# Kernel optimization log

Hardware: AMD Instinct MI355X
Metric: run time of the kernel (lower is better)

## Reference

```python
import jax, jax.numpy as jnp
import numpy as np

N_PROPOSALS = 100000
N_LABELS = 256
IOU_THRESHOLD = 0.5
FPS = 25.0


def setup_inputs() -> dict:
    key = jax.random.key(0)
    k1, k2, k3, k4, k5 = jax.random.split(key, 5)
    conf = jax.random.uniform(k1, (N_PROPOSALS,), dtype=jnp.float32)
    p_start = jax.random.uniform(k2, (N_PROPOSALS,), dtype=jnp.float32) * 2500.0  # frames
    p_len = jax.random.uniform(k3, (N_PROPOSALS,), dtype=jnp.float32) * 250.0 + 1.0
    proposals = jnp.stack([conf, p_start, p_start + p_len], axis=1)  # [N,3]
    l_start = jax.random.uniform(k4, (N_LABELS,), dtype=jnp.float32) * 100.0  # seconds
    l_len = jax.random.uniform(k5, (N_LABELS,), dtype=jnp.float32) * 10.0 + 0.5
    labels = jnp.stack([l_start, l_start + l_len], axis=1)  # [M,2]
    return {"proposals": proposals, "labels": labels}


def _iou_matrix(proposals, labels):
    # iou_with_anchors, vectorized over proposals (rows) x labels (cols)
    a_min = proposals[:, 1] / FPS  # [N] seconds
    a_max = proposals[:, 2] / FPS
    b_min = labels[:, 0]  # [M]
    b_max = labels[:, 1]
    inter = jnp.clip(
        jnp.minimum(a_max[:, None], b_max[None, :])
        - jnp.maximum(a_min[:, None], b_min[None, :]),
        0.0,
    )  # [N,M]
    union = (a_max - a_min)[:, None] - inter + (b_max - b_min)[None, :]
    return inter / union


def _greedy_tp(ious, iou_threshold):
    # Faithful greedy assignment: each proposal (in original order) claims the
    # first (lowest-index) still-undetected label it overlaps above threshold.
    over = ious > iou_threshold  # [N,M] bool

    def step(detected, row):
        pot = row & (~detected)  # [M]
        is_tp = pot.any()
        j = jnp.argmax(pot)  # first True (or 0 if none; guarded by is_tp)
        detected = detected.at[j].set(detected[j] | is_tp)
        return detected, is_tp

    _, is_TP = jax.lax.scan(step, jnp.zeros((ious.shape[1],), dtype=bool), over)
    return is_TP  # [N] bool


def reference(proposals, labels):
    n_labels = labels.shape[0]
    ious = _iou_matrix(proposals, labels)  # [N,M]
    is_TP = _greedy_tp(ious, IOU_THRESHOLD)  # [N]

    confidence = proposals[:, 0]
    # stable descending sort by confidence (matches torch sort(stable, descending))
    order = jnp.argsort(-confidence, stable=True)
    tp = is_TP[order].astype(jnp.float32)

    acc_TP = jnp.cumsum(tp)  # [N]
    denom = jnp.arange(1, tp.shape[0] + 1, dtype=jnp.float32)  # acc_TP + acc_FP
    precision = acc_TP / denom
    recall = acc_TP / jnp.float32(n_labels)

    # curve = [[1,0]] ++ flip(curve): x = recall, y = precision
    x = jnp.concatenate([jnp.ones((1,), jnp.float32), recall[::-1]])
    y = jnp.concatenate([jnp.zeros((1,), jnp.float32), precision[::-1]])
    y_max = jax.lax.cummax(y, axis=0)  # running max including current point
    ap = jnp.sum((x[:-1] - x[1:]) * y_max[:-1])
    return ap
```

## Files before the change

kernel.cpp:

```cpp
#include <hip/hip_runtime.h>
#include <stdint.h>

#define N_PROP 100000
#define N_LAB  256
#define NW     8
#define CHUNK  256
#define NCHUNK 391
#define NCH_P  392
#define N_PAD  (NCHUNK * CHUNK)
#define RANK_BLOCKS 128

#define OFF_MASKS   0
#define OFF_CHUNKOR (N_PAD * NW * 4)
#define OFF_KEYS    (OFF_CHUNKOR + NCHUNK * NW * 4)
#define OFF_TPCNT   (OFF_KEYS + N_LAB * 8)
#define OFF_CTRL    (OFF_TPCNT + 16)
#define CTRL_INTS 261

#define FIRST_PEND(j_i, w0, w1, w2, w3)         \
  {                                             \
    j_i = -1;                                   \
    if (w3) j_i = 192 + (__ffsll(w3) - 1);      \
    if (w2) j_i = 128 + (__ffsll(w2) - 1);      \
    if (w1) j_i = 64 + (__ffsll(w1) - 1);       \
    if (w0) j_i = (__ffsll(w0) - 1);            \
  }

__global__ __launch_bounds__(512) void k_masks(
    const float* __restrict__ prop, const float* __restrict__ lab,
    uint32_t* __restrict__ masks, uint32_t* __restrict__ chunkOR,
    int* __restrict__ ctrl) {
  __shared__ float4 s_lab[N_LAB];
  __shared__ uint32_t s_or[NW];
  const int t = threadIdx.x;
  const int h = t >> 8;
  const int q = t & 255;
  if (t < N_LAB) {
    const float bmn = lab[2 * t], bmx = lab[2 * t + 1];
    s_lab[t] = make_float4(bmn, bmx, bmx - bmn, 0.0f);
  }
  if (t < NW) s_or[t] = 0u;
  if (blockIdx.x == 0) {
    for (int z = t; z < CTRL_INTS; z += 512) ctrl[z] = 0;
  }
  __syncthreads();

  const int i = blockIdx.x * 256 + q;
  uint32_t m0 = 0u, m1 = 0u, m2 = 0u, m3 = 0u;

  if (i < N_PROP) {
    const float ps = prop[3 * i + 1], pe = prop[3 * i + 2];
    const float amin = ps / 25.0f;
    const float amax = pe / 25.0f;
    const float alen = amax - amin;
    const int j0 = h << 7;
#pragma unroll 4
    for (int jj = 0; jj < 128; ++jj) {
      const float4 L = s_lab[j0 + jj];
      float inter = fminf(amax, L.y) - fmaxf(amin, L.x);
      inter = fmaxf(inter, 0.0f);
      const float uni = (alen - inter) + L.z;
      const bool pred =
          __builtin_fmaf(2.0f, inter, -uni) > uni * 0x1p-25f;
      if (pred) {
        const uint32_t b = 1u << (jj & 31);
        const int w = jj >> 5;
        m0 |= (w == 0) ? b : 0u;  m1 |= (w == 1) ? b : 0u;
        m2 |= (w == 2) ? b : 0u;  m3 |= (w == 3) ? b : 0u;
      }
    }
  }

  *reinterpret_cast<uint4*>(&masks[(size_t)i * NW + h * 4]) =
      make_uint4(m0, m1, m2, m3);

  if (m0 | m1 | m2 | m3) {
    const int wb = h * 4;
    if (m0) atomicOr(&s_or[wb + 0], m0);
    if (m1) atomicOr(&s_or[wb + 1], m1);
    if (m2) atomicOr(&s_or[wb + 2], m2);
    if (m3) atomicOr(&s_or[wb + 3], m3);
  }
  __syncthreads();
  if (t < NW) chunkOR[blockIdx.x * NW + t] = s_or[t];
}

#define FLAG_LANE(CC, FVAR)                                                 \
  FVAR = (s_orT[0 * NCH_P + (CC)] & ~D0) | (s_orT[1 * NCH_P + (CC)] & ~D1) |\
         (s_orT[2 * NCH_P + (CC)] & ~D2) | (s_orT[3 * NCH_P + (CC)] & ~D3) |\
         (s_orT[4 * NCH_P + (CC)] & ~D4) | (s_orT[5 * NCH_P + (CC)] & ~D5) |\
         (s_orT[6 * NCH_P + (CC)] & ~D6) | (s_orT[7 * NCH_P + (CC)] & ~D7);

#define FIND_NEXT(C0, RES)                                                  \
  {                                                                         \
    const int start_ = (C0);              \
    RES = -1;                                                               \
    for (int c_ = start_; c_ < NCHUNK; c_ += 64) {                          \
      const int cc_ = c_ + lane;                                            \
      uint32_t f_ = 0u;                                                     \
      if (cc_ < NCHUNK) { FLAG_LANE(cc_, f_); }                             \
      const unsigned long long bal_ = __ballot(f_ != 0u);                   \
      if (bal_ != 0ull) { RES = c_ + (__ffsll(bal_) - 1); break; }          \
    }                                                                       \
  }

#define ISSUE(CH, R0A, R0B, R1A, R1B, R2A, R2B, R3A, R3B)                   \
  {                                                                         \
    const uint4* qm_ =                                                      \
        reinterpret_cast<const uint4*>(&masks[(size_t)(CH) * CHUNK * NW]);  \
    const int l2_ = lane * 2;                                               \
    R0A = qm_[l2_];       R0B = qm_[l2_ + 1];                               \
    R1A = qm_[128 + l2_]; R1B = qm_[128 + l2_ + 1];                         \
    R2A = qm_[256 + l2_]; R2B = qm_[256 + l2_ + 1];                         \
    R3A = qm_[384 + l2_]; R3B = qm_[384 + l2_ + 1];                         \
  }

#define PENDW(VA, VB)                                                       \
    w0 = ((unsigned long long)(VA.y & ~D1) << 32) |                         \
         (unsigned long long)(uint32_t)(VA.x & ~D0);                        \
    w1 = ((unsigned long long)(VA.w & ~D3) << 32) |                         \
         (unsigned long long)(uint32_t)(VA.z & ~D2);                        \
    w2 = ((unsigned long long)(VB.y & ~D5) << 32) |                         \
         (unsigned long long)(uint32_t)(VB.x & ~D4);                        \
    w3 = ((unsigned long long)(VB.w & ~D7) << 32) |                         \
         (unsigned long long)(uint32_t)(VB.z & ~D6);

#define DRAIN64B(BASE, VA, VB)                                              \
  {                                                                         \
    unsigned long long w0, w1, w2, w3;                                      \
    PENDW(VA, VB)                                                           \
    int j_i;                                                                \
    FIRST_PEND(j_i, w0, w1, w2, w3);                                        \
    while (true) {                                                          \
      const unsigned long long bal = __ballot(j_i >= 0);                    \
      if (bal == 0ull) break;                                               \
      ++epoch;                                                              \
      const unsigned my_ = ((unsigned)epoch << 8) | (63u ^ (unsigned)lane); \
      if (j_i >= 0) atomicMax(&s_own[j_i], my_);                            \
      __threadfence_block();                                                \
      const bool won_ = (j_i >= 0) && (s_own[j_i] == my_);                  \
      const unsigned long long lostb = __ballot((j_i >= 0) && !won_);       \
      const int fl_ = (lostb != 0ull) ? (__ffsll(lostb) - 1) : 64;          \
      const bool com_ = won_ && (lane < fl_);                               \
      const unsigned long long cbal = __ballot(com_);                       \
      if (com_) {                                                           \
        atomicOr(&s_D[j_i >> 5], 1u << (j_i & 31));                         \
        const int pos_ = T + __popcll(cbal & ((1ull << lane) - 1ull));      \
        if (pos_ < N_LAB) s_tpi[pos_] = (BASE) + lane;                      \
      }                                                                     \
      T += __popcll(cbal);                                                  \
      __threadfence_block();                                                \
      D0 = s_D[0]; D1 = s_D[1]; D2 = s_D[2]; D3 = s_D[3];                   \
      D4 = s_D[4]; D5 = s_D[5]; D6 = s_D[6]; D7 = s_D[7];                   \
      if (T >= N_LAB) break;                                                \
      if (com_) {                                                           \
        j_i = -1;                                 \
      } else if (j_i >= 0) {                     \
        PENDW(VA, VB)                                                       \
        FIRST_PEND(j_i, w0, w1, w2, w3);                                    \
      }                                                                     \
    }                                                                       \
  }

#define COPY_BA                                                             \
  a0A = b0A; a0B = b0B; a1A = b1A; a1B = b1B;                               \
  a2A = b2A; a2B = b2B; a3A = b3A; a3B = b3B;

__global__ __launch_bounds__(256) void k_scanrank(
    const uint32_t* __restrict__ masks, const uint32_t* __restrict__ chunkOR,
    const float* __restrict__ prop,
    unsigned long long* keys, int* tp_cnt, int* ctrl, float* out) {
  __shared__ uint32_t s_orT[NW * NCH_P];
  __shared__ uint32_t s_own[N_LAB];
  __shared__ uint32_t s_D[NW];
  __shared__ int s_tpi[N_LAB];
  __shared__ int s_T;
  __shared__ int s_last;
  __shared__ unsigned long long s_key[N_LAB];
  __shared__ unsigned long long s_srt[N_LAB];
  __shared__ int s_hist[N_LAB + 1];
  __shared__ int s_a[N_LAB + 1];
  __shared__ int s_b[N_LAB + 1];
  __shared__ int s_p[N_LAB];
  const int t = threadIdx.x;
  const int bid = blockIdx.x;
  int* hist = &ctrl[4];

  if (bid == 0) {
    s_own[t] = 0u;
    if (t < NW) s_D[t] = 0u;
    for (int f = t; f < NCHUNK * NW; f += 256)
      s_orT[(f & 7) * NCH_P + (f >> 3)] = chunkOR[f];
    __syncthreads();

    if (t < 64) {
      const int lane = t;
      uint32_t D0 = 0, D1 = 0, D2 = 0, D3 = 0, D4 = 0, D5 = 0, D6 = 0, D7 = 0;
      int T = 0;
      int epoch = 0;
      uint4 a0A, a0B, a1A, a1B, a2A, a2B, a3A, a3B;
      uint4 b0A, b0B, b1A, b1B, b2A, b2B, b3A, b3B;

      int cur;
      FIND_NEXT(0, cur);
      if (cur >= 0) { ISSUE(cur, a0A, a0B, a1A, a1B, a2A, a2B, a3A, a3B); }
      while (cur >= 0) {
        int nxt;
        FIND_NEXT(cur + 1, nxt);
        if (nxt >= 0) { ISSUE(nxt, b0A, b0B, b1A, b1B, b2A, b2B, b3A, b3B); }

        DRAIN64B(cur * CHUNK + 0,   a0A, a0B);
        DRAIN64B(cur * CHUNK + 64,  a1A, a1B);
        DRAIN64B(cur * CHUNK + 128, a2A, a2B);
        DRAIN64B(cur * CHUNK + 192, a3A, a3B);

        if (T >= N_LAB) break;
        while (nxt >= 0) {
          uint32_t fu;
          FLAG_LANE(nxt, fu);
          if (fu != 0u) break;
          FIND_NEXT(nxt + 1, nxt);
          if (nxt >= 0) { ISSUE(nxt, b0A, b0B, b1A, b1B, b2A, b2B, b3A, b3B); }
        }
        cur = nxt;
        if (cur >= 0) { COPY_BA }
      }
      if (lane == 0) s_T = (T < N_LAB) ? T : N_LAB;
    }
    __syncthreads();

    const int T = s_T;
    unsigned long long k = ~0ull;
    if (t < T) {
      const int it = s_tpi[t];
      const unsigned cb = __float_as_uint(prop[3 * it]);
      k = ((unsigned long long)cb << 32) |
          (unsigned long long)(0xFFFFFFFFu - (unsigned)it);
    }
    s_key[t] = k;
    s_srt[t] = ~0ull;
    __syncthreads();
    int pos = 0;
    for (int s = 0; s < N_LAB; ++s) pos += (s_key[s] < k) ? 1 : 0;
    if (t < T) s_srt[pos] = k;
    __syncthreads();
    keys[t] = s_srt[t];
    if (t == 0) tp_cnt[0] = T;
    __syncthreads();
    __threadfence();
    if (t == 0)
      __hip_atomic_store(&ctrl[0], 1, __ATOMIC_RELEASE,
                         __HIP_MEMORY_SCOPE_AGENT);
  } else {
    if (t == 0) {
      while (__hip_atomic_load(&ctrl[0], __ATOMIC_ACQUIRE,
                               __HIP_MEMORY_SCOPE_AGENT) == 0)
        __builtin_amdgcn_s_sleep(127);
    }
    __syncthreads();
    __threadfence();
  }

  s_key[t] = keys[t];
  s_hist[t] = 0;
  if (t == 0) s_hist[N_LAB] = 0;
  __syncthreads();

  for (int i = bid * 256 + t; i < N_PROP; i += RANK_BLOCKS * 256) {
    const unsigned cb = __float_as_uint(prop[3 * i]);
    const unsigned long long k =
        ((unsigned long long)cb << 32) |
        (unsigned long long)(0xFFFFFFFFu - (unsigned)i);
    int p = 0;
#pragma unroll
    for (int s = 256; s > 0; s >>= 1) {
      const int cand = p + s;
      if (cand <= N_LAB && s_key[cand - 1] < k) p = cand;
    }
    atomicAdd(&s_hist[p], 1);
  }
  __syncthreads();
  if (s_hist[t] != 0) atomicAdd(&hist[t], s_hist[t]);
  if (t == 0 && s_hist[N_LAB] != 0) atomicAdd(&hist[N_LAB], s_hist[N_LAB]);

  __threadfence();
  if (t == 0)
    s_last = (atomicAdd(&ctrl[1], 1) == RANK_BLOCKS - 1) ? 1 : 0;
  __syncthreads();
  if (!s_last) return;
  __threadfence();

  int T = tp_cnt[0];
  T = (T < 0) ? 0 : ((T > N_LAB) ? N_LAB : T);
  s_a[t] = atomicAdd(&hist[t], 0);
  if (t == 0) s_a[N_LAB] = atomicAdd(&hist[N_LAB], 0);
  __syncthreads();
  int* src = s_a;
  int* dst = s_b;
#pragma unroll
  for (int s = 1; s <= N_LAB; s <<= 1) {
    const int v = src[t] + ((t + s <= N_LAB) ? src[t + s] : 0);
    const int v256 = (t == 0) ? src[N_LAB] : 0;
    __syncthreads();
    dst[t] = v;
    if (t == 0) dst[N_LAB] = v256;
    __syncthreads();
    int* tmp = src; src = dst; dst = tmp;
  }
  if (t < T) s_p[(T - 1) - t] = 1 + src[t + 1];
  __syncthreads();
  if (t == 0) {
    float m = 0.0f, sum = 0.0f;
    for (int i = T - 1; i >= 0; --i) {
      const float prec = (float)(i + 1) / (float)s_p[i];
      m = fmaxf(m, prec);
      if (s_p[i] >= 2) sum += m * 0.00390625f;
    }
    out[0] = sum;
  }
}

extern "C" void kernel_launch(void* const* d_in, const int* in_sizes, int n_in,
                              void* d_out, int out_size, void* d_ws,
                              size_t ws_size, hipStream_t stream) {
  (void)in_sizes; (void)n_in; (void)out_size; (void)ws_size;
  const float* prop = (const float*)d_in[0];
  const float* lab  = (const float*)d_in[1];
  uint8_t* ws = (uint8_t*)d_ws;
  uint32_t* masks  = (uint32_t*)(ws + OFF_MASKS);
  uint32_t* chOR   = (uint32_t*)(ws + OFF_CHUNKOR);
  unsigned long long* keys = (unsigned long long*)(ws + OFF_KEYS);
  int*      tp_cnt = (int*)(ws + OFF_TPCNT);
  int*      ctrl   = (int*)(ws + OFF_CTRL);
  float*    out    = (float*)d_out;

  k_masks  <<<dim3(NCHUNK),      dim3(512), 0, stream>>>(prop, lab, masks,
                                                         chOR, ctrl);
  k_scanrank<<<dim3(RANK_BLOCKS), dim3(256), 0, stream>>>(masks, chOR, prop,
                                                          keys, tp_cnt, ctrl,
                                                          out);
}
```

Measured before the change: 103.2 us.

## Split scan and rank into separate kernels, drop in-kernel spin-wait and block fences

The single-block greedy scan and sort moves into its own one-block kernel, and the histogram-rank plus AP pass becomes a third kernel launched afterwards. This replaces the global release/acquire flag and the spin-waiting of 127 blocks with kernel-boundary ordering. Control-word zeroing moves into the scan kernel, and the ctrl counter index changes. Two __threadfence_block calls are also removed from the drain loop. The price is an extra launch and reliance on LDS atomic ordering without explicit fences.

```diff
diff --git a/kernel.cpp b/kernel.cpp
--- a/kernel.cpp
+++ b/kernel.cpp
@@ -15,7 +15,6 @@
 #define OFF_KEYS    (OFF_CHUNKOR + NCHUNK * NW * 4)
 #define OFF_TPCNT   (OFF_KEYS + N_LAB * 8)
 #define OFF_CTRL    (OFF_TPCNT + 16)
-#define CTRL_INTS 261
 
 #define FIRST_PEND(j_i, w0, w1, w2, w3)         \
   {                                             \
@@ -28,8 +27,7 @@
 
 __global__ __launch_bounds__(512) void k_masks(
     const float* __restrict__ prop, const float* __restrict__ lab,
-    uint32_t* __restrict__ masks, uint32_t* __restrict__ chunkOR,
-    int* __restrict__ ctrl) {
+    uint32_t* __restrict__ masks, uint32_t* __restrict__ chunkOR) {
   __shared__ float4 s_lab[N_LAB];
   __shared__ uint32_t s_or[NW];
   const int t = threadIdx.x;
@@ -40,9 +38,6 @@
     s_lab[t] = make_float4(bmn, bmx, bmx - bmn, 0.0f);
   }
   if (t < NW) s_or[t] = 0u;
-  if (blockIdx.x == 0) {
-    for (int z = t; z < CTRL_INTS; z += 512) ctrl[z] = 0;
-  }
   __syncthreads();
 
   const int i = blockIdx.x * 256 + q;
@@ -137,7 +132,6 @@
       ++epoch;                                                              \
       const unsigned my_ = ((unsigned)epoch << 8) | (63u ^ (unsigned)lane); \
       if (j_i >= 0) atomicMax(&s_own[j_i], my_);                            \
-      __threadfence_block();                                                \
       const bool won_ = (j_i >= 0) && (s_own[j_i] == my_);                  \
       const unsigned long long lostb = __ballot((j_i >= 0) && !won_);       \
       const int fl_ = (lostb != 0ull) ? (__ffsll(lostb) - 1) : 64;          \
@@ -149,7 +143,6 @@
         if (pos_ < N_LAB) s_tpi[pos_] = (BASE) + lane;                      \
       }                                                                     \
       T += __popcll(cbal);                                                  \
-      __threadfence_block();                                                \
       D0 = s_D[0]; D1 = s_D[1]; D2 = s_D[2]; D3 = s_D[3];                   \
       D4 = s_D[4]; D5 = s_D[5]; D6 = s_D[6]; D7 = s_D[7];                   \
       if (T >= N_LAB) break;                                                \
@@ -166,107 +159,101 @@
   a0A = b0A; a0B = b0B; a1A = b1A; a1B = b1B;                               \
   a2A = b2A; a2B = b2B; a3A = b3A; a3B = b3B;
 
-__global__ __launch_bounds__(256) void k_scanrank(
+__global__ __launch_bounds__(256) void k_scansort(
     const uint32_t* __restrict__ masks, const uint32_t* __restrict__ chunkOR,
     const float* __restrict__ prop,
-    unsigned long long* keys, int* tp_cnt, int* ctrl, float* out) {
+    unsigned long long* __restrict__ keys, int* __restrict__ tp_cnt,
+    int* __restrict__ ctrl) {
   __shared__ uint32_t s_orT[NW * NCH_P];
   __shared__ uint32_t s_own[N_LAB];
   __shared__ uint32_t s_D[NW];
   __shared__ int s_tpi[N_LAB];
   __shared__ int s_T;
-  __shared__ int s_last;
   __shared__ unsigned long long s_key[N_LAB];
   __shared__ unsigned long long s_srt[N_LAB];
+  const int t = threadIdx.x;
+
+  if (t == 0) ctrl[2] = 0;
+  for (int z = t; z <= N_LAB; z += 256) ctrl[4 + z] = 0;
+  s_own[t] = 0u;
+  if (t < NW) s_D[t] = 0u;
+
+  for (int f = t; f < NCHUNK * NW; f += 256)
+    s_orT[(f & 7) * NCH_P + (f >> 3)] = chunkOR[f];
+  __syncthreads();
+
+  if (t < 64) {
+    const int lane = t;
+    uint32_t D0 = 0, D1 = 0, D2 = 0, D3 = 0, D4 = 0, D5 = 0, D6 = 0, D7 = 0;
+    int T = 0;
+    int epoch = 0;
+    uint4 a0A, a0B, a1A, a1B, a2A, a2B, a3A, a3B;
+    uint4 b0A, b0B, b1A, b1B, b2A, b2B, b3A, b3B;
+
+    int cur;
+    FIND_NEXT(0, cur);
+    if (cur >= 0) { ISSUE(cur, a0A, a0B, a1A, a1B, a2A, a2B, a3A, a3B); }
+    while (cur >= 0) {
+      int nxt;
+      FIND_NEXT(cur + 1, nxt);
+      if (nxt >= 0) { ISSUE(nxt, b0A, b0B, b1A, b1B, b2A, b2B, b3A, b3B); }
+
+      DRAIN64B(cur * CHUNK + 0,   a0A, a0B);
+      DRAIN64B(cur * CHUNK + 64,  a1A, a1B);
+      DRAIN64B(cur * CHUNK + 128, a2A, a2B);
+      DRAIN64B(cur * CHUNK + 192, a3A, a3B);
+
+      if (T >= N_LAB) break;
+      while (nxt >= 0) {
+        uint32_t fu;
+        FLAG_LANE(nxt, fu);
+        if (fu != 0u) break;
+        FIND_NEXT(nxt + 1, nxt);
+        if (nxt >= 0) { ISSUE(nxt, b0A, b0B, b1A, b1B, b2A, b2B, b3A, b3B); }
+      }
+      cur = nxt;
+      if (cur >= 0) { COPY_BA }
+    }
+    if (lane == 0) s_T = (T < N_LAB) ? T : N_LAB;
+  }
+  __syncthreads();
+
+  const int T = s_T;
+  unsigned long long k = ~0ull;
+  if (t < T) {
+    const int it = s_tpi[t];
+    const unsigned cb = __float_as_uint(prop[3 * it]);
+    k = ((unsigned long long)cb << 32) |
+        (unsigned long long)(0xFFFFFFFFu - (unsigned)it);
+  }
+  s_key[t] = k;
+  s_srt[t] = ~0ull;
+  __syncthreads();
+  int pos = 0;
+  for (int s = 0; s < N_LAB; ++s) pos += (s_key[s] < k) ? 1 : 0;
+  if (t < T) s_srt[pos] = k;
+  __syncthreads();
+  keys[t] = s_srt[t];
+  if (t == 0) tp_cnt[0] = T;
+}
+
+__global__ __launch_bounds__(256) void k_rankap(
+    const float* __restrict__ prop, const unsigned long long* __restrict__ keys,
+    const int* __restrict__ tp_cnt, int* ctrl, float* __restrict__ out) {
+  __shared__ unsigned long long s_key[N_LAB];
   __shared__ int s_hist[N_LAB + 1];
+  __shared__ int s_last;
   __shared__ int s_a[N_LAB + 1];
   __shared__ int s_b[N_LAB + 1];
   __shared__ int s_p[N_LAB];
   const int t = threadIdx.x;
-  const int bid = blockIdx.x;
   int* hist = &ctrl[4];
-
-  if (bid == 0) {
-    s_own[t] = 0u;
-    if (t < NW) s_D[t] = 0u;
-    for (int f = t; f < NCHUNK * NW; f += 256)
-      s_orT[(f & 7) * NCH_P + (f >> 3)] = chunkOR[f];
-    __syncthreads();
-
-    if (t < 64) {
-      const int lane = t;
-      uint32_t D0 = 0, D1 = 0, D2 = 0, D3 = 0, D4 = 0, D5 = 0, D6 = 0, D7 = 0;
-      int T = 0;
-      int epoch = 0;
-      uint4 a0A, a0B, a1A, a1B, a2A, a2B, a3A, a3B;
-      uint4 b0A, b0B, b1A, b1B, b2A, b2B, b3A, b3B;
-
-      int cur;
-      FIND_NEXT(0, cur);
-      if (cur >= 0) { ISSUE(cur, a0A, a0B, a1A, a1B, a2A, a2B, a3A, a3B); }
-      while (cur >= 0) {
-        int nxt;
-        FIND_NEXT(cur + 1, nxt);
-        if (nxt >= 0) { ISSUE(nxt, b0A, b0B, b1A, b1B, b2A, b2B, b3A, b3B); }
-
-        DRAIN64B(cur * CHUNK + 0,   a0A, a0B);
-        DRAIN64B(cur * CHUNK + 64,  a1A, a1B);
-        DRAIN64B(cur * CHUNK + 128, a2A, a2B);
-        DRAIN64B(cur * CHUNK + 192, a3A, a3B);
-
-        if (T >= N_LAB) break;
-        while (nxt >= 0) {
-          uint32_t fu;
-          FLAG_LANE(nxt, fu);
-          if (fu != 0u) break;
-          FIND_NEXT(nxt + 1, nxt);
-          if (nxt >= 0) { ISSUE(nxt, b0A, b0B, b1A, b1B, b2A, b2B, b3A, b3B); }
-        }
-        cur = nxt;
-        if (cur >= 0) { COPY_BA }
-      }
-      if (lane == 0) s_T = (T < N_LAB) ? T : N_LAB;
-    }
-    __syncthreads();
-
-    const int T = s_T;
-    unsigned long long k = ~0ull;
-    if (t < T) {
-      const int it = s_tpi[t];
-      const unsigned cb = __float_as_uint(prop[3 * it]);
-      k = ((unsigned long long)cb << 32) |
-          (unsigned long long)(0xFFFFFFFFu - (unsigned)it);
-    }
-    s_key[t] = k;
-    s_srt[t] = ~0ull;
-    __syncthreads();
-    int pos = 0;
-    for (int s = 0; s < N_LAB; ++s) pos += (s_key[s] < k) ? 1 : 0;
-    if (t < T) s_srt[pos] = k;
-    __syncthreads();
-    keys[t] = s_srt[t];
-    if (t == 0) tp_cnt[0] = T;
-    __syncthreads();
-    __threadfence();
-    if (t == 0)
-      __hip_atomic_store(&ctrl[0], 1, __ATOMIC_RELEASE,
-                         __HIP_MEMORY_SCOPE_AGENT);
-  } else {
-    if (t == 0) {
-      while (__hip_atomic_load(&ctrl[0], __ATOMIC_ACQUIRE,
-                               __HIP_MEMORY_SCOPE_AGENT) == 0)
-        __builtin_amdgcn_s_sleep(127);
-    }
-    __syncthreads();
-    __threadfence();
-  }
-
   s_key[t] = keys[t];
   s_hist[t] = 0;
   if (t == 0) s_hist[N_LAB] = 0;
   __syncthreads();
 
-  for (int i = bid * 256 + t; i < N_PROP; i += RANK_BLOCKS * 256) {
+  for (int i = blockIdx.x * 256 + t; i < N_PROP; i += RANK_BLOCKS * 256) {
     const unsigned cb = __float_as_uint(prop[3 * i]);
     const unsigned long long k =
         ((unsigned long long)cb << 32) |
@@ -285,7 +272,7 @@
 
   __threadfence();
   if (t == 0)
-    s_last = (atomicAdd(&ctrl[1], 1) == RANK_BLOCKS - 1) ? 1 : 0;
+    s_last = (atomicAdd(&ctrl[2], 1) == RANK_BLOCKS - 1) ? 1 : 0;
   __syncthreads();
   if (!s_last) return;
   __threadfence();
@@ -334,9 +321,9 @@
   int*      ctrl   = (int*)(ws + OFF_CTRL);
   float*    out    = (float*)d_out;
 
-  k_masks  <<<dim3(NCHUNK),      dim3(512), 0, stream>>>(prop, lab, masks,
-                                                         chOR, ctrl);
-  k_scanrank<<<dim3(RANK_BLOCKS), dim3(256), 0, stream>>>(masks, chOR, prop,
-                                                          keys, tp_cnt, ctrl,
-                                                          out);
+  k_masks   <<<dim3(NCHUNK),      dim3(512), 0, stream>>>(prop, lab, masks, chOR);
+  k_scansort<<<dim3(1),           dim3(256), 0, stream>>>(masks, chOR, prop,
+                                                          keys, tp_cnt, ctrl);
+  k_rankap  <<<dim3(RANK_BLOCKS), dim3(256), 0, stream>>>(prop, keys, tp_cnt,
+                                                          ctrl, out);
 }
```

New measurement: 94.18 us (median of 2 runs). 8.7% less time.
